# Kernel optimization log

Measured on AMD Instinct MI355X. Metric: run time of the kernel, lower is better.

## Reference

```python
import jax, jax.numpy as jnp
import numpy as np
import math

D_MODEL = 1024
N_HEADS = 16
D_KV = 64
ROPE_BASE = 10000.0


def absmean_quantize_weight(w):
    # ternary absmean quantization: scale = mean(|w|), round-to-nearest-even, clamp to {-1,0,1}
    scale = jnp.mean(jnp.abs(w))
    return jnp.clip(jnp.round(w / scale), -1.0, 1.0) * scale


def quantize_activation(x, num_bits=8):
    qmax = 2.0 ** (num_bits - 1) - 1.0  # 127
    scale = jnp.max(jnp.abs(x)) / qmax
    return jnp.clip(jnp.round(x / scale), -qmax, qmax) * scale


def bitlinear(x, w):
    return quantize_activation(x) @ absmean_quantize_weight(w).T


def rope_tables(seq_len, dim, dtype):
    inv_freq = 1.0 / (ROPE_BASE ** (jnp.arange(0, dim, 2, dtype=jnp.float32) / dim))
    t = jnp.arange(seq_len, dtype=jnp.float32)
    freqs = jnp.einsum('i,j->ij', t, inv_freq)        # [S, dim/2]
    emb = jnp.concatenate([freqs, freqs], axis=-1)    # [S, dim]
    # broadcast shape [1, 1, S, dim]
    return jnp.cos(emb)[None, None].astype(dtype), jnp.sin(emb)[None, None].astype(dtype)


def rotate_half(x):
    x1, x2 = jnp.split(x, 2, axis=-1)
    return jnp.concatenate([-x2, x1], axis=-1)


def setup_inputs() -> dict:
    key = jax.random.key(0)
    ks = jax.random.split(key, 5)
    B, S = 2, 2048
    bound = 1.0 / math.sqrt(D_MODEL)  # kaiming-uniform-ish scale
    return {
        'hidden_states': jax.random.normal(ks[0], (B, S, D_MODEL), dtype=jnp.float32),
        'Wq': jax.random.uniform(ks[1], (N_HEADS * D_KV, D_MODEL), jnp.float32, -bound, bound),
        'Wk': jax.random.uniform(ks[2], (N_HEADS * D_KV, D_MODEL), jnp.float32, -bound, bound),
        'Wv': jax.random.uniform(ks[3], (N_HEADS * D_KV, D_MODEL), jnp.float32, -bound, bound),
        'Wo': jax.random.uniform(ks[4], (D_MODEL, N_HEADS * D_KV), jnp.float32, -bound, bound),
    }


def reference(hidden_states, Wq, Wk, Wv, Wo):
    B, S, _ = hidden_states.shape
    inner = N_HEADS * D_KV

    def split_heads(x):
        return x.reshape(B, S, N_HEADS, D_KV).transpose(0, 2, 1, 3)  # [B,H,S,Dk]

    q = split_heads(bitlinear(hidden_states, Wq))
    k = split_heads(bitlinear(hidden_states, Wk))
    v = split_heads(bitlinear(hidden_states, Wv))

    cos, sin = rope_tables(S, D_KV, q.dtype)
    q = q * cos + rotate_half(q) * sin
    k = k * cos + rotate_half(k) * sin

    scores = jnp.einsum('bhqd,bhkd->bhqk', q, k) / math.sqrt(D_KV)
    attn_weights = jax.nn.softmax(scores.astype(jnp.float32), axis=-1).astype(scores.dtype)
    # dropout p=0.0 / eval mode -> identity
    attn_output = jnp.einsum('bhqk,bhkd->bhqd', attn_weights, v)
    attn_output = attn_output.transpose(0, 2, 1, 3).reshape(B, S, inner)
    attn_output = bitlinear(attn_output, Wo)
    return attn_output, attn_weights
```

## Files before the change

kernel.cpp:

```cpp
#include <hip/hip_runtime.h>
#include <math.h>

typedef __attribute__((ext_vector_type(8))) short short8;
typedef __attribute__((ext_vector_type(4))) float f32x4;
typedef __attribute__((ext_vector_type(4))) int i32x4;
typedef __attribute__((ext_vector_type(4))) unsigned int u32x4;

#define DEV __device__ __forceinline__

static constexpr int B_ = 2, S_ = 2048, H_ = 16, D_ = 64, DM_ = 1024;
static constexpr int BH_ = B_ * H_;
static constexpr int NQ_ = B_ * S_;
static constexpr size_t OUT0_ELEMS = (size_t)NQ_ * DM_;
static constexpr float LOG2E = 1.4426950408889634f;
static constexpr float A2 = 0.125f * 1.4426950408889634f;

static constexpr size_t OFF_PMAXX = 256;
static constexpr size_t OFF_PSUM  = 1280;
static constexpr size_t OFF_PMAXA = 4096;
static constexpr size_t OFF_K2M   = 12288;
static constexpr size_t OFF_COS   = 16384;
static constexpr size_t OFF_SIN   = OFF_COS + (size_t)S_ * 32 * 4;
static constexpr size_t OFF_Q2    = OFF_SIN + (size_t)S_ * 32 * 4;
static constexpr size_t OFF_XQ    = (size_t)1 << 20;
static constexpr size_t OFF_WQ8   = OFF_XQ   + (size_t)NQ_ * DM_;
static constexpr size_t OFF_QB    = OFF_WQ8  + (size_t)4096 * 1024;
static constexpr size_t OFF_KB    = OFF_QB   + (size_t)BH_ * S_ * D_ * 2;
static constexpr size_t OFF_VT    = OFF_KB   + (size_t)BH_ * S_ * D_ * 2;
static constexpr size_t OFF_APRE  = OFF_VT   + (size_t)BH_ * D_ * S_ * 2;
static constexpr size_t OFF_AQ    = OFF_APRE + (size_t)NQ_ * DM_ * 4;
static constexpr size_t WS_NEED   = OFF_AQ   + (size_t)NQ_ * DM_;

DEV unsigned short f2bf(float f) {
  unsigned u = __builtin_bit_cast(unsigned, f);
  return (unsigned short)((u + 0x7fffu + ((u >> 16) & 1u)) >> 16);
}
DEV float bf2f(unsigned short h) {
  unsigned u = ((unsigned)h) << 16;
  return __builtin_bit_cast(float, u);
}
DEV void gload16(const void* g, void* l) {
  __builtin_amdgcn_global_load_lds((const __attribute__((address_space(1))) unsigned int*)g,
                                   (__attribute__((address_space(3))) unsigned int*)l, 16, 0, 0);
}
DEV int q8pack(float4 v, float sc, float lim) {
  int i0 = (int)fminf(fmaxf(rintf(v.x / sc), -lim), lim);
  int i1 = (int)fminf(fmaxf(rintf(v.y / sc), -lim), lim);
  int i2 = (int)fminf(fmaxf(rintf(v.z / sc), -lim), lim);
  int i3 = (int)fminf(fmaxf(rintf(v.w / sc), -lim), lim);
  return (int)(((unsigned)(i0 & 255)) | ((unsigned)(i1 & 255) << 8) |
               ((unsigned)(i2 & 255) << 16) | ((unsigned)(i3 & 255) << 24));
}

__global__ void k_reduce6(const float* __restrict__ x, const float* __restrict__ w0,
                          const float* __restrict__ w1, const float* __restrict__ w2,
                          const float* __restrict__ w3, float* __restrict__ pmaxx,
                          float* __restrict__ psum, float* __restrict__ cosT,
                          float* __restrict__ sinT) {
  __shared__ float red[256];
  const int y = blockIdx.y;
  if (y == 5) {
    const int i0 = (blockIdx.x * 256 + threadIdx.x) * 2;
#pragma unroll
    for (int t = 0; t < 2; ++t) {
      const int i = i0 + t;
      const int s = i >> 5, f = i & 31;
      double inv = pow(10000.0, -(double)(2 * f) / 64.0);
      float th = (float)s * (float)inv;
      cosT[i] = (float)cos((double)th);
      sinT[i] = (float)sin((double)th);
    }
    return;
  }
  if (y == 0) {
    const float4* xv = (const float4*)x;
    float mv = 0.f;
    for (int i = blockIdx.x * 256 + threadIdx.x; i < 1048576; i += 128 * 256) {
      float4 v = xv[i];
      mv = fmaxf(mv, fmaxf(fmaxf(fabsf(v.x), fabsf(v.y)), fmaxf(fabsf(v.z), fabsf(v.w))));
    }
    red[threadIdx.x] = mv;
    __syncthreads();
    for (int st = 128; st > 0; st >>= 1) {
      if ((int)threadIdx.x < st) red[threadIdx.x] = fmaxf(red[threadIdx.x], red[threadIdx.x + st]);
      __syncthreads();
    }
    if (threadIdx.x == 0) pmaxx[blockIdx.x] = red[0];
  } else {
    const float* wsrc = (y == 1) ? w0 : (y == 2) ? w1 : (y == 3) ? w2 : w3;
    const float4* xv = (const float4*)wsrc;
    float s = 0.f;
    for (int i = blockIdx.x * 256 + threadIdx.x; i < 262144; i += 128 * 256) {
      float4 v = xv[i];
      s += fabsf(v.x) + fabsf(v.y) + fabsf(v.z) + fabsf(v.w);
    }
    red[threadIdx.x] = s;
    __syncthreads();
    for (int st = 128; st > 0; st >>= 1) {
      if ((int)threadIdx.x < st) red[threadIdx.x] += red[threadIdx.x + st];
      __syncthreads();
    }
    if (threadIdx.x == 0) psum[(y - 1) * 128 + blockIdx.x] = red[0];
  }
}

__global__ void k_finalize1(float* __restrict__ wsf, float* __restrict__ k2m) {
  const float* pmax = wsf + OFF_PMAXX / 4;
  const float* psum = wsf + OFF_PSUM / 4;
  const int w = threadIdx.x >> 6, l = threadIdx.x & 63;
  float s = psum[w * 128 + l] + psum[w * 128 + 64 + l];
#pragma unroll
  for (int off = 1; off < 64; off <<= 1) s += __shfl_xor(s, off);
  if (l == 0) wsf[1 + w] = s / 1048576.0f;
  if (w == 0) {
    float m = fmaxf(pmax[l], pmax[l + 64]);
#pragma unroll
    for (int off = 1; off < 64; off <<= 1) m = fmaxf(m, __shfl_xor(m, off));
    if (l == 0) wsf[0] = m / 127.0f;
  }
  if (threadIdx.x < 32) k2m[threadIdx.x] = 0.f;
}

__global__ void k_quant_all(const float* __restrict__ x, const float* __restrict__ w0,
                            const float* __restrict__ w1, const float* __restrict__ w2,
                            const float* __restrict__ w3, const float* __restrict__ scal,
                            signed char* __restrict__ xq, signed char* __restrict__ wq) {
  const int bid = blockIdx.x;
  if (bid < 4096) {
    const int i = bid * 256 + threadIdx.x;
    const float sc = scal[0];
    ((int*)xq)[i] = q8pack(((const float4*)x)[i], sc, 127.f);
  } else {
    const int wi = bid - 4096;
    const int y = wi >> 10;
    const int i = (wi & 1023) * 256 + threadIdx.x;
    const float* src = (y == 0) ? w0 : (y == 1) ? w1 : (y == 2) ? w2 : w3;
    const float sc = scal[1 + y];
    ((int*)(wq + (size_t)y * 1048576))[i] = q8pack(((const float4*)src)[i], sc, 1.f);
  }
}

__global__ void k_quant_a8(const float* __restrict__ x, const float* __restrict__ pmaxa,
                           float* __restrict__ wsf, signed char* __restrict__ out) {
  __shared__ float red[256];
  float m = 0.f;
  for (int k = threadIdx.x; k < 1024; k += 256) m = fmaxf(m, pmaxa[k]);
  red[threadIdx.x] = m;
  __syncthreads();
  for (int st = 128; st > 0; st >>= 1) {
    if ((int)threadIdx.x < st) red[threadIdx.x] = fmaxf(red[threadIdx.x], red[threadIdx.x + st]);
    __syncthreads();
  }
  const float sc = red[0] / 127.0f;
  if (blockIdx.x == 0 && threadIdx.x == 0) wsf[5] = sc;
  const int i = blockIdx.x * 256 + threadIdx.x;
  ((int*)out)[i] = q8pack(((const float4*)x)[i], sc, 127.f);
}

template <int MODE>
__launch_bounds__(256, 3)
__global__ void k_gemm(const signed char* __restrict__ Ag, const signed char* __restrict__ Bg,
                       const float* __restrict__ scal, const float* __restrict__ cosT,
                       const float* __restrict__ sinT, unsigned short* __restrict__ Qb,
                       unsigned short* __restrict__ Kb, unsigned short* __restrict__ Vt,
                       float* __restrict__ q2t, float* __restrict__ k2m, float* __restrict__ Co) {
  constexpr int TM = (MODE == 0) ? 128 : 64;
  constexpr int MT = TM / 32;
  constexpr int NBX = (MODE == 0) ? 24 : 8;
  constexpr int CPX = (MODE == 0) ? 96 : 64;
  __shared__ alignas(16) unsigned char As[3][TM * 64];
  __shared__ alignas(16) unsigned char Bs[3][128 * 64];
  const int w = threadIdx.x >> 6, l = threadIdx.x & 63;

  const int bid = (int)blockIdx.x + (int)blockIdx.y * NBX;
  const int nl = (bid & 7) * CPX + (bid >> 3);
  const int mbase = (nl / NBX) * TM, nbase = (nl % NBX) * 128;

  const i32x4 izero = {0, 0, 0, 0};
  i32x4 acc[MT][4];
#pragma unroll
  for (int a = 0; a < MT; ++a)
#pragma unroll
    for (int b = 0; b < 4; ++b) acc[a][b] = izero;

  const int csrc = (l & 3) ^ ((l >> 2) & 3) ^ ((l >> 4) & 3);
  const int r16 = l >> 2;

  auto stage = [&](int kt, int buf) {
#pragma unroll
    for (int i = 0; i < TM / 64; ++i) {
      const int chunk = w * (TM / 64) + i;
      const int grow = mbase + chunk * 16 + r16;
      gload16(Ag + (size_t)grow * 1024 + kt * 64 + csrc * 16, &As[buf][chunk << 10]);
    }
#pragma unroll
    for (int i = 0; i < 2; ++i) {
      const int chunk = w * 2 + i;
      const int grow = nbase + chunk * 16 + r16;
      gload16(Bg + (size_t)grow * 1024 + kt * 64 + csrc * 16, &Bs[buf][chunk << 10]);
    }
  };
  auto wait_lps = [&]() {
    if constexpr (MODE == 0) asm volatile("s_waitcnt vmcnt(4)" ::: "memory");
    else asm volatile("s_waitcnt vmcnt(3)" ::: "memory");
  };

  const int rA0 = (w >> 1) * (TM / 2) + (l & 15);
  const int rB0 = (w & 1) * 64 + (l & 15);
  const int kc = l >> 4;
  auto compute = [&](int buf) {
    const unsigned char* Ab = &As[buf][0];
    const unsigned char* Bb = &Bs[buf][0];
    i32x4 af[MT], bf[4];
#pragma unroll
    for (int t = 0; t < MT; ++t) {
      const int ra = rA0 + t * 16;
      af[t] = *(const i32x4*)(Ab + ra * 64 + ((kc ^ (ra & 3) ^ ((ra >> 2) & 3)) << 4));
    }
#pragma unroll
    for (int t = 0; t < 4; ++t) {
      const int rb = rB0 + t * 16;
      bf[t] = *(const i32x4*)(Bb + rb * 64 + ((kc ^ (rb & 3) ^ ((rb >> 2) & 3)) << 4));
    }
#pragma unroll
    for (int mt = 0; mt < MT; ++mt)
#pragma unroll
      for (int nt = 0; nt < 4; ++nt)
        acc[mt][nt] = __builtin_amdgcn_mfma_i32_16x16x64_i8(af[mt], bf[nt], acc[mt][nt], 0, 0, 0);
  };

  stage(0, 0);
  stage(1, 1);
  wait_lps();
  __syncthreads();
  for (int kt = 0; kt < 16; ++kt) {
    const int cur = kt % 3;
    if (kt < 14) {
      stage(kt + 2, (kt + 2) % 3);
      compute(cur);
      wait_lps();
    } else {
      compute(cur);
      asm volatile("s_waitcnt vmcnt(0)" ::: "memory");
    }
    __syncthreads();
  }

  if constexpr (MODE == 0) {
    const int wm = w >> 1, wn = w & 1;
    const int gcolbase = nbase + wn * 64;
    const int section = gcolbase >> 10;
    const int h = (gcolbase & 1023) >> 6;
    const float sc = scal[0] * scal[1 + section];
    const int growbase = mbase + wm * 64;
    if (section < 2) {
      unsigned short* Outb = (section == 0) ? Qb : Kb;
      float wmax = 0.f;
#pragma unroll
      for (int mt = 0; mt < MT; ++mt)
#pragma unroll
        for (int r = 0; r < 4; ++r) {
          const int grow = growbase + mt * 16 + ((l >> 4) << 2) + r;
          const int b = grow >> 11, s = grow & 2047;
          const size_t ob = ((size_t)(b * 16 + h) * 2048 + s) * 64;
          float rsq = 0.f;
#pragma unroll
          for (int nt = 0; nt < 2; ++nt) {
            const int d = nt * 16 + (l & 15);
            const float v1 = (float)acc[mt][nt][r] * sc;
            const float v2 = (float)acc[mt][nt + 2][r] * sc;
            const float cv = cosT[s * 32 + d];
            const float sv = sinT[s * 32 + d];
            const unsigned short h1 = f2bf(v1 * cv - v2 * sv);
            const unsigned short h2 = f2bf(v2 * cv + v1 * sv);
            Outb[ob + d] = h1;
            Outb[ob + d + 32] = h2;
            const float o1 = bf2f(h1), o2 = bf2f(h2);
            rsq += o1 * o1 + o2 * o2;
          }
#pragma unroll
          for (int off = 1; off < 16; off <<= 1) rsq += __shfl_xor(rsq, off);
          if (section == 0) {
            if ((l & 15) == 0) q2t[(size_t)(b * 16 + h) * 2048 + s] = rsq;
          } else {
            wmax = fmaxf(wmax, rsq);
          }
        }
      if (section == 1) {
        wmax = fmaxf(wmax, __shfl_xor(wmax, 16));
        wmax = fmaxf(wmax, __shfl_xor(wmax, 32));
        if (l == 0) {
          const int b = growbase >> 11;
          atomicMax((unsigned int*)&k2m[b * 16 + h], __builtin_bit_cast(unsigned int, wmax));
        }
      }
    } else {
      unsigned short* Tw = (unsigned short*)(&As[0][0]) + w * 2176;
#pragma unroll
      for (int h0 = 0; h0 < 2; ++h0) {
#pragma unroll
        for (int mh = 0; mh < 2; ++mh) {
          const int mt = h0 * 2 + mh;
#pragma unroll
          for (int r = 0; r < 4; ++r) {
            const int srow = mh * 16 + ((l >> 4) << 2) + r;
#pragma unroll
            for (int nt = 0; nt < 4; ++nt)
              Tw[srow * 68 + nt * 16 + (l & 15)] = f2bf((float)acc[mt][nt][r] * sc);
          }
        }
        asm volatile("s_waitcnt lgkmcnt(0)" ::: "memory");
        __builtin_amdgcn_sched_barrier(0);
        const int i = l & 15, dq = l >> 4;
#pragma unroll
        for (int d0 = 0; d0 < 16; ++d0) {
          const int d = d0 * 4 + dq;
          const unsigned a = Tw[(2 * i) * 68 + d];
          const unsigned b2 = Tw[(2 * i + 1) * 68 + d];
          const int sglob = growbase + h0 * 32 + 2 * i;
          const int b = sglob >> 11, s = sglob & 2047;
          *(unsigned*)(Vt + ((size_t)((b * 16 + h) * 64 + d) * 2048 + s)) = a | (b2 << 16);
        }
        asm volatile("s_waitcnt lgkmcnt(0)" ::: "memory");
        __builtin_amdgcn_sched_barrier(0);
      }
    }
  } else {
    const float sc = scal[4] * scal[5];
#pragma unroll
    for (int mt = 0; mt < MT; ++mt)
#pragma unroll
      for (int r = 0; r < 4; ++r) {
        const int grow = mbase + (w >> 1) * (TM / 2) + mt * 16 + ((l >> 4) << 2) + r;
#pragma unroll
        for (int nt = 0; nt < 4; ++nt) {
          const int gcol = nbase + (w & 1) * 64 + nt * 16 + (l & 15);
          Co[(size_t)grow * 1024 + gcol] = (float)acc[mt][nt][r] * sc;
        }
      }
  }
}

__launch_bounds__(256, 3)
__global__ void k_attn(const unsigned short* __restrict__ Qb, const unsigned short* __restrict__ Kb,
                       const unsigned short* __restrict__ Vt, const float* __restrict__ q2t,
                       const float* __restrict__ k2m, float* __restrict__ Wout,
                       float* __restrict__ Apre, float* __restrict__ pmaxa) {
  __shared__ alignas(16) char smem[48 * 1024];

  const int bid = (int)blockIdx.x;
  const int swz = ((bid & 7) << 7) | (bid >> 3);
  const int bh = swz >> 5, qt = swz & 31;
  const int w = threadIdx.x >> 6, l = threadIdx.x & 63;

  const unsigned short* Kg = Kb + (size_t)bh * S_ * D_;
  const unsigned short* Vg = Vt + (size_t)bh * D_ * S_;

  short8 aq[2];
  {
    const int qrow_f = qt * 64 + w * 16 + (l & 15);
    const unsigned short* qp = Qb + (size_t)bh * S_ * D_ + (size_t)qrow_f * D_ + ((l >> 4) << 3);
    aq[0] = *(const short8*)qp;
    aq[1] = *(const short8*)(qp + 32);
  }

  float cb[4];
  {
    const float km = k2m[bh];
#pragma unroll
    for (int r = 0; r < 4; ++r) {
      const int qr = qt * 64 + w * 16 + ((l >> 4) << 2) + r;
      cb[r] = sqrtf(q2t[(size_t)bh * 2048 + qr] * km) * 0.125f * LOG2E;
    }
  }

  const f32x4 vzero = {0.f, 0.f, 0.f, 0.f};
  const int kxor = ((l & 7) << 4) ^ ((l >> 3) << 4);
  const int lxor = ((l << 4) ^ ((l >> 3) << 4));

  auto stageKbuf = [&](int kb, char* dst) {
    const char* baseK = (const char*)(Kg + (size_t)kb * 64 * D_);
#pragma unroll
    for (int i = 0; i < 2; ++i) {
      int j = (w << 1) + i;
      gload16(baseK + (j << 10) + lxor, dst + (j << 10));
    }
  };
  auto qktbuf = [&](const char* Kbase, f32x4* sa) {
#pragma unroll
    for (int c = 0; c < 2; ++c) {
      const int colb = (c << 6) + ((l >> 4) << 4);
      short8 bk[4];
#pragma unroll
      for (int ct = 0; ct < 4; ++ct) {
        const int rb = (ct << 4) + (l & 15);
        bk[ct] = *(const short8*)(Kbase + rb * 128 + (colb ^ ((rb & 7) << 4)));
      }
#pragma unroll
      for (int ct = 0; ct < 4; ++ct)
        sa[ct] = __builtin_amdgcn_mfma_f32_16x16x32_bf16(aq[c], bk[ct], sa[ct], 0, 0, 0);
    }
  };

  float lt[4] = {0.f, 0.f, 0.f, 0.f};
  stageKbuf(0, smem);
  stageKbuf(1, smem + 8192);
  asm volatile("s_waitcnt vmcnt(2)" ::: "memory");
  __syncthreads();
  for (int kb = 0; kb < 32; ++kb) {
    const int cur = kb % 3;
    if (kb < 30) stageKbuf(kb + 2, smem + ((kb + 2) % 3) * 8192);
    f32x4 sa[4];
#pragma unroll
    for (int t = 0; t < 4; ++t) sa[t] = vzero;
    qktbuf(smem + cur * 8192, sa);
#pragma unroll
    for (int r = 0; r < 4; ++r) {
      lt[r] += exp2f(fmaf(sa[0][r], A2, -cb[r])) + exp2f(fmaf(sa[1][r], A2, -cb[r])) +
               exp2f(fmaf(sa[2][r], A2, -cb[r])) + exp2f(fmaf(sa[3][r], A2, -cb[r]));
    }
    if (kb < 31) {
      asm volatile("s_waitcnt vmcnt(2)" ::: "memory");
    } else {
      asm volatile("s_waitcnt vmcnt(0)" ::: "memory");
    }
    __syncthreads();
  }

  float rl[4];
#pragma unroll
  for (int r = 0; r < 4; ++r) {
    float s = lt[r];
#pragma unroll
    for (int off = 1; off < 16; off <<= 1) s += __shfl_xor(s, off);
    rl[r] = 1.0f / s;
  }

  f32x4 oacc[4];
#pragma unroll
  for (int t = 0; t < 4; ++t) oacc[t] = vzero;
  char* KsB = smem;
  char* VhsB = smem + 16384;
  float* Pw = (float*)(smem + 32768) + w * 1024;
  const size_t wb0 = (size_t)bh * S_ * S_;

  auto stageB = [&](int kb, int buf) {
    const char* baseK = (const char*)(Kg + (size_t)kb * 64 * D_);
#pragma unroll
    for (int i = 0; i < 2; ++i) {
      int j = (w << 1) + i;
      gload16(baseK + (j << 10) + lxor, KsB + buf * 8192 + (j << 10));
      const size_t voff = (size_t)(j * 8 + (l >> 3)) * (S_ * 2) + (size_t)kb * 128 + kxor;
      gload16((const char*)Vg + voff, VhsB + buf * 8192 + (j << 10));
    }
  };

  stageB(0, 0);
  asm volatile("s_waitcnt vmcnt(0)" ::: "memory");
  __syncthreads();
  for (int kb = 0; kb < 32; ++kb) {
    const int cur = kb & 1;
    if (kb < 31) stageB(kb + 1, cur ^ 1);

    f32x4 sa[4];
#pragma unroll
    for (int t = 0; t < 4; ++t) sa[t] = vzero;
    qktbuf(KsB + cur * 8192, sa);

#pragma unroll
    for (int ct = 0; ct < 4; ++ct) {
#pragma unroll
      for (int r = 0; r < 4; ++r) {
        const float p = exp2f(fmaf(sa[ct][r], A2, -cb[r])) * rl[r];
        const int prow = ((l >> 4) << 2) + r;
        const int pbyte = (ct * 16 + (l & 15)) << 2;
        *(float*)((char*)Pw + prow * 256 + (pbyte ^ ((prow & 7) << 4))) = p;
      }
    }

    {
      const size_t wrow0 = wb0 + (size_t)(qt * 64 + w * 16) * S_ + (size_t)kb * 64;
#pragma unroll
      for (int i = 0; i < 4; ++i) {
        const int prow = (i << 2) + (l >> 4);
        const int cb2 = (l & 15) << 4;
        const f32x4 f = *(const f32x4*)((const char*)Pw + prow * 256 + (cb2 ^ ((prow & 7) << 4)));
        __builtin_nontemporal_store(
            f, (f32x4*)(Wout + wrow0 + (size_t)prow * S_ + ((l & 15) << 2)));
      }
    }

#pragma unroll
    for (int c = 0; c < 2; ++c) {
      const int arow = l & 15;
      const int abyte = (c << 7) + ((l >> 4) << 5);
      const u32x4 u0 = *(const u32x4*)((const char*)Pw + arow * 256 + (abyte ^ ((arow & 7) << 4)));
      const u32x4 u1 =
          *(const u32x4*)((const char*)Pw + arow * 256 + ((abyte + 16) ^ ((arow & 7) << 4)));
      short8 ph, pl;
#pragma unroll
      for (int j = 0; j < 4; ++j) {
        const unsigned ua = u0[j], ub = u1[j];
        ph[j] = (short)(ua >> 16);
        ph[4 + j] = (short)(ub >> 16);
        const float da = __builtin_bit_cast(float, ua) -
                         __builtin_bit_cast(float, ua & 0xffff0000u);
        const float db = __builtin_bit_cast(float, ub) -
                         __builtin_bit_cast(float, ub & 0xffff0000u);
        pl[j] = (short)(__builtin_bit_cast(unsigned, da) >> 16);
        pl[4 + j] = (short)(__builtin_bit_cast(unsigned, db) >> 16);
      }
      const int colb = (c << 6) + ((l >> 4) << 4);
#pragma unroll
      for (int dt = 0; dt < 4; ++dt) {
        const int rv = (dt << 4) + (l & 15);
        const short8 vh =
            *(const short8*)(VhsB + cur * 8192 + rv * 128 + (colb ^ ((rv & 7) << 4)));
        oacc[dt] = __builtin_amdgcn_mfma_f32_16x16x32_bf16(ph, vh, oacc[dt], 0, 0, 0);
        oacc[dt] = __builtin_amdgcn_mfma_f32_16x16x32_bf16(pl, vh, oacc[dt], 0, 0, 0);
      }
    }
    asm volatile("s_waitcnt vmcnt(4)" ::: "memory");
    __syncthreads();
  }

  const int b = bh >> 4, h = bh & 15;
  float am = 0.f;
#pragma unroll
  for (int dt = 0; dt < 4; ++dt)
#pragma unroll
    for (int r = 0; r < 4; ++r) {
      const int qr = qt * 64 + w * 16 + ((l >> 4) << 2) + r;
      Apre[(size_t)(b * S_ + qr) * DM_ + h * 64 + dt * 16 + (l & 15)] = oacc[dt][r];
      am = fmaxf(am, fabsf(oacc[dt][r]));
    }
#pragma unroll
  for (int off = 1; off < 64; off <<= 1) am = fmaxf(am, __shfl_xor(am, off));
  __syncthreads();
  float* red = (float*)smem;
  if (l == 0) red[w] = am;
  __syncthreads();
  if (threadIdx.x == 0)
    pmaxa[bid] = fmaxf(fmaxf(red[0], red[1]), fmaxf(red[2], red[3]));
}

extern "C" void kernel_launch(void* const* d_in, const int* in_sizes, int n_in, void* d_out,
                              int out_size, void* d_ws, size_t ws_size, hipStream_t stream) {
  const float* hidden = (const float*)d_in[0];
  const float* Wq = (const float*)d_in[1];
  const float* Wk = (const float*)d_in[2];
  const float* Wv = (const float*)d_in[3];
  const float* Wo = (const float*)d_in[4];
  float* out0 = (float*)d_out;
  float* out1 = out0 + OUT0_ELEMS;

  if (ws_size < WS_NEED) return;

  char* ws = (char*)d_ws;
  float* wsf = (float*)ws;
  float* pmaxx = (float*)(ws + OFF_PMAXX);
  float* psum = (float*)(ws + OFF_PSUM);
  float* pmaxa = (float*)(ws + OFF_PMAXA);
  float* k2mp = (float*)(ws + OFF_K2M);
  float* cosT = (float*)(ws + OFF_COS);
  float* sinT = (float*)(ws + OFF_SIN);
  float* q2p = (float*)(ws + OFF_Q2);
  signed char* xq8 = (signed char*)(ws + OFF_XQ);
  signed char* wq8 = (signed char*)(ws + OFF_WQ8);
  unsigned short* Qbp = (unsigned short*)(ws + OFF_QB);
  unsigned short* Kbp = (unsigned short*)(ws + OFF_KB);
  unsigned short* Vtp = (unsigned short*)(ws + OFF_VT);
  float* apre = (float*)(ws + OFF_APRE);
  signed char* aq8 = (signed char*)(ws + OFF_AQ);

  k_reduce6<<<dim3(128, 6), 256, 0, stream>>>(hidden, Wq, Wk, Wv, Wo, pmaxx, psum, cosT, sinT);
  k_finalize1<<<1, 256, 0, stream>>>(wsf, k2mp);
  k_quant_all<<<8192, 256, 0, stream>>>(hidden, Wq, Wk, Wv, Wo, wsf, xq8, wq8);
  k_gemm<0><<<dim3(24, 32), 256, 0, stream>>>(xq8, wq8, wsf, cosT, sinT, Qbp, Kbp, Vtp, q2p, k2mp,
                                              nullptr);
  k_attn<<<1024, 256, 0, stream>>>(Qbp, Kbp, Vtp, q2p, k2mp, out1, apre, pmaxa);
  k_quant_a8<<<4096, 256, 0, stream>>>(apre, pmaxa, wsf, aq8);
  k_gemm<1><<<dim3(8, 64), 256, 0, stream>>>(aq8, wq8 + (size_t)3 * 1048576, wsf, nullptr, nullptr,
                                             nullptr, nullptr, nullptr, nullptr, nullptr, out0);
  (void)in_sizes; (void)n_in; (void)out_size;
}
```

Measured before the change: 223.4 us.

## Process two query tiles per attention block, overlapping second pass-A with first pass-B

Each attention block now handles two 64-row query tiles. The row-sum pass for the second tile is fused into the K/V streaming loop of the first tile's output pass, so one K stream is shared. The goal is to cut redundant K reads and halve the grid. The cost is half as many blocks (512), which lowers occupancy and parallelism on a large GPU and adds register pressure. The output GEMM also now uses nontemporal stores, and the pmax reduction is shortened to match the new grid size.

```diff
diff --git a/kernel.cpp b/kernel.cpp
--- a/kernel.cpp
+++ b/kernel.cpp
@@ -144,7 +144,7 @@
                            float* __restrict__ wsf, signed char* __restrict__ out) {
   __shared__ float red[256];
   float m = 0.f;
-  for (int k = threadIdx.x; k < 1024; k += 256) m = fmaxf(m, pmaxa[k]);
+  for (int k = threadIdx.x; k < 512; k += 256) m = fmaxf(m, pmaxa[k]);
   red[threadIdx.x] = m;
   __syncthreads();
   for (int st = 128; st > 0; st >>= 1) {
@@ -335,7 +335,8 @@
 #pragma unroll
         for (int nt = 0; nt < 4; ++nt) {
           const int gcol = nbase + (w & 1) * 64 + nt * 16 + (l & 15);
-          Co[(size_t)grow * 1024 + gcol] = (float)acc[mt][nt][r] * sc;
+          __builtin_nontemporal_store((float)acc[mt][nt][r] * sc,
+                                      Co + (size_t)grow * 1024 + gcol);
         }
       }
   }
@@ -349,28 +350,32 @@
   __shared__ alignas(16) char smem[48 * 1024];
 
   const int bid = (int)blockIdx.x;
-  const int swz = ((bid & 7) << 7) | (bid >> 3);
-  const int bh = swz >> 5, qt = swz & 31;
+  const int swz = ((bid & 7) << 6) | (bid >> 3);
+  const int bh = swz >> 4, qp = swz & 15;
+  const int qt0 = qp * 2, qt1 = qp * 2 + 1;
   const int w = threadIdx.x >> 6, l = threadIdx.x & 63;
 
   const unsigned short* Kg = Kb + (size_t)bh * S_ * D_;
   const unsigned short* Vg = Vt + (size_t)bh * D_ * S_;
 
-  short8 aq[2];
+  short8 aq0[2], aq1[2];
   {
-    const int qrow_f = qt * 64 + w * 16 + (l & 15);
-    const unsigned short* qp = Qb + (size_t)bh * S_ * D_ + (size_t)qrow_f * D_ + ((l >> 4) << 3);
-    aq[0] = *(const short8*)qp;
-    aq[1] = *(const short8*)(qp + 32);
-  }
-
-  float cb[4];
+    const int qr = qt0 * 64 + w * 16 + (l & 15);
+    const unsigned short* qp_ = Qb + (size_t)bh * S_ * D_ + (size_t)qr * D_ + ((l >> 4) << 3);
+    aq0[0] = *(const short8*)qp_;
+    aq0[1] = *(const short8*)(qp_ + 32);
+    aq1[0] = *(const short8*)(qp_ + 64 * D_);
+    aq1[1] = *(const short8*)(qp_ + 64 * D_ + 32);
+  }
+
+  float cb0[4], cb1[4];
   {
     const float km = k2m[bh];
 #pragma unroll
     for (int r = 0; r < 4; ++r) {
-      const int qr = qt * 64 + w * 16 + ((l >> 4) << 2) + r;
-      cb[r] = sqrtf(q2t[(size_t)bh * 2048 + qr] * km) * 0.125f * LOG2E;
+      const int qr = qt0 * 64 + w * 16 + ((l >> 4) << 2) + r;
+      cb0[r] = sqrtf(q2t[(size_t)bh * 2048 + qr] * km) * 0.125f * LOG2E;
+      cb1[r] = sqrtf(q2t[(size_t)bh * 2048 + qr + 64] * km) * 0.125f * LOG2E;
     }
   }
 
@@ -386,7 +391,7 @@
       gload16(baseK + (j << 10) + lxor, dst + (j << 10));
     }
   };
-  auto qktbuf = [&](const char* Kbase, f32x4* sa) {
+  auto qktbuf = [&](const char* Kbase, const short8* aq, f32x4* sa) {
 #pragma unroll
     for (int c = 0; c < 2; ++c) {
       const int colb = (c << 6) + ((l >> 4) << 4);
@@ -402,7 +407,7 @@
     }
   };
 
-  float lt[4] = {0.f, 0.f, 0.f, 0.f};
+  float lt0[4] = {0.f, 0.f, 0.f, 0.f};
   stageKbuf(0, smem);
   stageKbuf(1, smem + 8192);
   asm volatile("s_waitcnt vmcnt(2)" ::: "memory");
@@ -413,11 +418,11 @@
     f32x4 sa[4];
 #pragma unroll
     for (int t = 0; t < 4; ++t) sa[t] = vzero;
-    qktbuf(smem + cur * 8192, sa);
+    qktbuf(smem + cur * 8192, aq0, sa);
 #pragma unroll
     for (int r = 0; r < 4; ++r) {
-      lt[r] += exp2f(fmaf(sa[0][r], A2, -cb[r])) + exp2f(fmaf(sa[1][r], A2, -cb[r])) +
-               exp2f(fmaf(sa[2][r], A2, -cb[r])) + exp2f(fmaf(sa[3][r], A2, -cb[r]));
+      lt0[r] += exp2f(fmaf(sa[0][r], A2, -cb0[r])) + exp2f(fmaf(sa[1][r], A2, -cb0[r])) +
+                exp2f(fmaf(sa[2][r], A2, -cb0[r])) + exp2f(fmaf(sa[3][r], A2, -cb0[r]));
     }
     if (kb < 31) {
       asm volatile("s_waitcnt vmcnt(2)" ::: "memory");
@@ -427,18 +432,15 @@
     __syncthreads();
   }
 
-  float rl[4];
+  float rl0[4];
 #pragma unroll
   for (int r = 0; r < 4; ++r) {
-    float s = lt[r];
+    float s = lt0[r];
 #pragma unroll
     for (int off = 1; off < 16; off <<= 1) s += __shfl_xor(s, off);
-    rl[r] = 1.0f / s;
-  }
-
-  f32x4 oacc[4];
-#pragma unroll
-  for (int t = 0; t < 4; ++t) oacc[t] = vzero;
+    rl0[r] = 1.0f / s;
+  }
+
   char* KsB = smem;
   char* VhsB = smem + 16384;
   float* Pw = (float*)(smem + 32768) + w * 1024;
@@ -454,30 +456,22 @@
       gload16((const char*)Vg + voff, VhsB + buf * 8192 + (j << 10));
     }
   };
-
-  stageB(0, 0);
-  asm volatile("s_waitcnt vmcnt(0)" ::: "memory");
-  __syncthreads();
-  for (int kb = 0; kb < 32; ++kb) {
-    const int cur = kb & 1;
-    if (kb < 31) stageB(kb + 1, cur ^ 1);
-
+  auto passB_tile = [&](int kb, int cur, int qt, const float* rl, const float* cbq,
+                        const short8* aq, f32x4* oacc) {
     f32x4 sa[4];
 #pragma unroll
     for (int t = 0; t < 4; ++t) sa[t] = vzero;
-    qktbuf(KsB + cur * 8192, sa);
-
+    qktbuf(KsB + cur * 8192, aq, sa);
 #pragma unroll
     for (int ct = 0; ct < 4; ++ct) {
 #pragma unroll
       for (int r = 0; r < 4; ++r) {
-        const float p = exp2f(fmaf(sa[ct][r], A2, -cb[r])) * rl[r];
+        const float p = exp2f(fmaf(sa[ct][r], A2, -cbq[r])) * rl[r];
         const int prow = ((l >> 4) << 2) + r;
         const int pbyte = (ct * 16 + (l & 15)) << 2;
         *(float*)((char*)Pw + prow * 256 + (pbyte ^ ((prow & 7) << 4))) = p;
       }
     }
-
     {
       const size_t wrow0 = wb0 + (size_t)(qt * 64 + w * 16) * S_ + (size_t)kb * 64;
 #pragma unroll
@@ -489,7 +483,6 @@
             f, (f32x4*)(Wout + wrow0 + (size_t)prow * S_ + ((l & 15) << 2)));
       }
     }
-
 #pragma unroll
     for (int c = 0; c < 2; ++c) {
       const int arow = l & 15;
@@ -520,17 +513,73 @@
         oacc[dt] = __builtin_amdgcn_mfma_f32_16x16x32_bf16(pl, vh, oacc[dt], 0, 0, 0);
       }
     }
+  };
+
+  f32x4 oacc[4];
+#pragma unroll
+  for (int t = 0; t < 4; ++t) oacc[t] = vzero;
+  float lt1[4] = {0.f, 0.f, 0.f, 0.f};
+
+  stageB(0, 0);
+  asm volatile("s_waitcnt vmcnt(0)" ::: "memory");
+  __syncthreads();
+  for (int kb = 0; kb < 32; ++kb) {
+    const int cur = kb & 1;
+    if (kb < 31) stageB(kb + 1, cur ^ 1);
+    {
+      f32x4 sa[4];
+#pragma unroll
+      for (int t = 0; t < 4; ++t) sa[t] = vzero;
+      qktbuf(KsB + cur * 8192, aq1, sa);
+#pragma unroll
+      for (int r = 0; r < 4; ++r) {
+        lt1[r] += exp2f(fmaf(sa[0][r], A2, -cb1[r])) + exp2f(fmaf(sa[1][r], A2, -cb1[r])) +
+                  exp2f(fmaf(sa[2][r], A2, -cb1[r])) + exp2f(fmaf(sa[3][r], A2, -cb1[r]));
+      }
+    }
+    passB_tile(kb, cur, qt0, rl0, cb0, aq0, oacc);
     asm volatile("s_waitcnt vmcnt(4)" ::: "memory");
     __syncthreads();
   }
 
+  float rl1[4];
+#pragma unroll
+  for (int r = 0; r < 4; ++r) {
+    float s = lt1[r];
+#pragma unroll
+    for (int off = 1; off < 16; off <<= 1) s += __shfl_xor(s, off);
+    rl1[r] = 1.0f / s;
+  }
+
   const int b = bh >> 4, h = bh & 15;
   float am = 0.f;
 #pragma unroll
   for (int dt = 0; dt < 4; ++dt)
 #pragma unroll
     for (int r = 0; r < 4; ++r) {
-      const int qr = qt * 64 + w * 16 + ((l >> 4) << 2) + r;
+      const int qr = qt0 * 64 + w * 16 + ((l >> 4) << 2) + r;
+      Apre[(size_t)(b * S_ + qr) * DM_ + h * 64 + dt * 16 + (l & 15)] = oacc[dt][r];
+      am = fmaxf(am, fabsf(oacc[dt][r]));
+    }
+#pragma unroll
+  for (int t = 0; t < 4; ++t) oacc[t] = vzero;
+
+  stageB(0, 0);
+  asm volatile("s_waitcnt vmcnt(0)" ::: "memory");
+  __syncthreads();
+  for (int kb = 0; kb < 32; ++kb) {
+    const int cur = kb & 1;
+    if (kb < 31) stageB(kb + 1, cur ^ 1);
+    passB_tile(kb, cur, qt1, rl1, cb1, aq1, oacc);
+    asm volatile("s_waitcnt vmcnt(4)" ::: "memory");
+    __syncthreads();
+  }
+
+#pragma unroll
+  for (int dt = 0; dt < 4; ++dt)
+#pragma unroll
+    for (int r = 0; r < 4; ++r) {
+      const int qr = qt1 * 64 + w * 16 + ((l >> 4) << 2) + r;
       Apre[(size_t)(b * S_ + qr) * DM_ + h * 64 + dt * 16 + (l & 15)] = oacc[dt][r];
       am = fmaxf(am, fabsf(oacc[dt][r]));
     }
@@ -578,7 +627,7 @@
   k_quant_all<<<8192, 256, 0, stream>>>(hidden, Wq, Wk, Wv, Wo, wsf, xq8, wq8);
   k_gemm<0><<<dim3(24, 32), 256, 0, stream>>>(xq8, wq8, wsf, cosT, sinT, Qbp, Kbp, Vtp, q2p, k2mp,
                                               nullptr);
-  k_attn<<<1024, 256, 0, stream>>>(Qbp, Kbp, Vtp, q2p, k2mp, out1, apre, pmaxa);
+  k_attn<<<512, 256, 0, stream>>>(Qbp, Kbp, Vtp, q2p, k2mp, out1, apre, pmaxa);
   k_quant_a8<<<4096, 256, 0, stream>>>(apre, pmaxa, wsf, aq8);
   k_gemm<1><<<dim3(8, 64), 256, 0, stream>>>(aq8, wq8 + (size_t)3 * 1048576, wsf, nullptr, nullptr,
                                              nullptr, nullptr, nullptr, nullptr, nullptr, out0);
```

Measured after the change: 226.1 us. No clear change (+1.2%).
